# Kernel tuning notes

Hardware: AMD Instinct MI355X
Metric: run time of the kernel (lower is better)

## Reference

```python
import jax, jax.numpy as jnp
import numpy as np

H, D_MODEL, DK, DV = 16, 1024, 64, 64
B, S = 4, 2048
LN_EPS = 1e-6
NEG = -1e9


def setup_inputs() -> dict:
    key = jax.random.key(0)
    ks = jax.random.split(key, 8)
    query = jax.random.normal(ks[0], (B, S, D_MODEL), dtype=jnp.float32)
    k_in = jax.random.normal(ks[1], (B, S, D_MODEL), dtype=jnp.float32)
    v_in = jax.random.normal(ks[2], (B, S, D_MODEL), dtype=jnp.float32)
    mask = jax.random.randint(ks[3], (B, S, S), 0, 2, dtype=jnp.int32)
    sc = 1.0 / np.sqrt(D_MODEL)
    w_qs = jax.random.normal(ks[4], (D_MODEL, H * DK), dtype=jnp.float32) * sc
    w_ks = jax.random.normal(ks[5], (D_MODEL, H * DK), dtype=jnp.float32) * sc
    w_vs = jax.random.normal(ks[6], (D_MODEL, H * DV), dtype=jnp.float32) * sc
    w_out = jax.random.normal(ks[7], (H * DV, D_MODEL), dtype=jnp.float32) * (1.0 / np.sqrt(H * DV))
    ln_g = jnp.ones((D_MODEL,), dtype=jnp.float32)
    ln_b = jnp.zeros((D_MODEL,), dtype=jnp.float32)
    return {"query": query, "key": k_in, "value": v_in, "mask": mask,
            "w_qs": w_qs, "w_ks": w_ks, "w_vs": w_vs, "w_out": w_out,
            "ln_g": ln_g, "ln_b": ln_b}


def reference(query, key, value, mask, w_qs, w_ks, w_vs, w_out, ln_g, ln_b):
    # projections -> [B, H, S, dk/dv]
    q = (query @ w_qs).reshape(B, S, H, DK).transpose(0, 2, 1, 3)
    k = (key @ w_ks).reshape(B, S, H, DK).transpose(0, 2, 1, 3)
    v = (value @ w_vs).reshape(B, S, H, DV).transpose(0, 2, 1, 3)
    scores = jnp.einsum('bhqd,bhkd->bhqk', q, k) / np.sqrt(DK)
    scores = jnp.where(mask[:, None, :, :] == 0, NEG, scores)
    p = jax.nn.softmax(scores, axis=-1)  # dropout = identity in eval
    x = jnp.einsum('bhqk,bhkd->bhqd', p, v)  # [B,H,S,DV]
    x = x.transpose(0, 2, 1, 3).reshape(B, S, H * DV)
    out = x @ w_out + query  # dropout identity, residual
    mu = out.mean(-1, keepdims=True)
    var = out.var(-1, keepdims=True)
    return (out - mu) / jnp.sqrt(var + LN_EPS) * ln_g + ln_b
```

## Files before the change

### kernel.cpp

```cpp
#include <hip/hip_runtime.h>

#define BB   4
#define SS   2048
#define HH   16
#define DM   1024
#define DKV  64
#define LNEPS 1e-6f

#define MD_BF16 0
#define MD_F32  1
#define MD_F16  2

typedef __attribute__((ext_vector_type(8))) short bf16x8;
typedef __attribute__((ext_vector_type(4))) float f32x4;
#define MFMA16(a,b,c) __builtin_amdgcn_mfma_f32_16x16x32_bf16(a,b,c,0,0,0)

__device__ __forceinline__ float2 unpack2(unsigned int u) {
    union { unsigned int i; float f; } a, b;
    a.i = u << 16;
    b.i = u & 0xffff0000u;
    return make_float2(a.f, b.f);
}
__device__ __forceinline__ unsigned short f2bf(float f) {
    union { float f; unsigned int i; } c; c.f = f;
    unsigned int u = c.i;
    unsigned int r = u + 0x7fffu + ((u >> 16) & 1u);
    return (unsigned short)(r >> 16);
}
__device__ __forceinline__ unsigned short f2bf_t(float f) {
    union { float f; unsigned int i; } c; c.f = f;
    return (unsigned short)(c.i >> 16);
}
__device__ __forceinline__ float h2f(unsigned int bits16) {
    unsigned short s = (unsigned short)bits16;
    _Float16 x;
    __builtin_memcpy(&x, &s, 2);
    return (float)x;
}
__device__ __forceinline__ void load8m(const void* p, int mode, size_t e0, float* o) {
    if (mode == MD_F32) {
        const float* f = (const float*)p + e0;
        float4 a = *(const float4*)f;
        float4 b = *(const float4*)(f + 4);
        o[0] = a.x; o[1] = a.y; o[2] = a.z; o[3] = a.w;
        o[4] = b.x; o[5] = b.y; o[6] = b.z; o[7] = b.w;
    } else {
        uint4 u = *(const uint4*)((const ushort*)p + e0);
        unsigned v[4] = {u.x, u.y, u.z, u.w};
        if (mode == MD_BF16) {
#pragma unroll
            for (int j = 0; j < 4; ++j) { float2 t = unpack2(v[j]); o[2*j] = t.x; o[2*j+1] = t.y; }
        } else {
#pragma unroll
            for (int j = 0; j < 4; ++j) { o[2*j] = h2f(v[j] & 0xFFFFu); o[2*j+1] = h2f(v[j] >> 16); }
        }
    }
}
__device__ __forceinline__ void load4m(const void* p, int mode, size_t e0, float* o) {
    if (mode == MD_F32) {
        float4 v = *(const float4*)((const float*)p + e0);
        o[0] = v.x; o[1] = v.y; o[2] = v.z; o[3] = v.w;
    } else {
        uint2 u = *(const uint2*)((const ushort*)p + e0);
        if (mode == MD_BF16) {
            float2 a = unpack2(u.x), b = unpack2(u.y);
            o[0] = a.x; o[1] = a.y; o[2] = b.x; o[3] = b.y;
        } else {
            o[0] = h2f(u.x & 0xFFFFu); o[1] = h2f(u.x >> 16);
            o[2] = h2f(u.y & 0xFFFFu); o[3] = h2f(u.y >> 16);
        }
    }
}
__device__ __forceinline__ float loadS(const void* p, int mode, size_t i) {
    if (mode == MD_F32) return ((const float*)p)[i];
    unsigned short u = ((const ushort*)p)[i];
    if (mode == MD_BF16) { union { unsigned i; float f; } c; c.i = (unsigned)u << 16; return c.f; }
    return h2f(u);
}

struct SniffArgs { const void* p[10]; int nhalf[10]; };

__global__ void sniff_all(SniffArgs a, int* __restrict__ modes) {
    __shared__ int cE, cO;
    const int slots[9] = {0, 1, 2, 4, 5, 6, 7, 8, 9};
    const int slot = slots[blockIdx.x];
    const ushort* p = (const ushort*)a.p[slot];
    const int nhalf = a.nhalf[slot];
    if (threadIdx.x == 0) { cE = 0; cO = 0; }
    __syncthreads();
    int e = 0, o = 0;
    for (int i = threadIdx.x; i < nhalf; i += 256) {
        unsigned ex = (p[i] >> 7) & 0xFFu;
        int hit = (ex < 100u || ex == 0xFFu) ? 1 : 0;
        if (i & 1) o += hit; else e += hit;
    }
    atomicAdd(&cE, e);
    atomicAdd(&cO, o);
    __syncthreads();
    if (threadIdx.x == 0) {
        int total = cE + cO;
        modes[slot] = (total < 48) ? MD_BF16 : ((cO * 4 < cE) ? MD_F32 : MD_F16);
    }
}

__global__ __launch_bounds__(256) void mpack(
    const int* __restrict__ mask, unsigned int* __restrict__ pm)
{
    const int w = blockIdx.x * 256 + threadIdx.x;
    const int* p = mask + (size_t)w * 32;
    unsigned int bits = 0u;
#pragma unroll
    for (int j = 0; j < 8; ++j) {
        int4 v = *(const int4*)(p + j * 4);
        bits |= (v.x ? 1u : 0u) << (4 * j);
        bits |= (v.y ? 1u : 0u) << (4 * j + 1);
        bits |= (v.z ? 1u : 0u) << (4 * j + 2);
        bits |= (v.w ? 1u : 0u) << (4 * j + 3);
    }
    pm[w] = bits;
}

__global__ __launch_bounds__(256) void wtrans(
    const void* __restrict__ W, ushort* __restrict__ Wt,
    const int* __restrict__ modes, int wslot)
{
    __shared__ ushort T[64][68];
    const int tid = threadIdx.x;
    const int m = modes[wslot];
    const int k0 = blockIdx.y * 64, n0 = blockIdx.x * 64;

    const int r = tid >> 2, c = (tid & 3) * 16;
    float t[4];
#pragma unroll
    for (int j = 0; j < 4; ++j) {
        load4m(W, m, (size_t)(k0 + r) * DM + n0 + c + 4 * j, t);
#pragma unroll
        for (int i = 0; i < 4; ++i) T[r][c + 4 * j + i] = f2bf(t[i]);
    }
    __syncthreads();

    const int rn = tid >> 2, ck = (tid & 3) * 16;
    union { ushort u[8]; uint4 v; } p0, p1;
#pragma unroll
    for (int j = 0; j < 8; ++j) { p0.u[j] = T[ck + j][rn]; p1.u[j] = T[ck + 8 + j][rn]; }
    ushort* op = &Wt[(size_t)(n0 + rn) * DM + k0 + ck];
    *(uint4*)op = p0.v;
    *(uint4*)(op + 8) = p1.v;
}

__global__ __launch_bounds__(256) void proj_mfma(
    const void* __restrict__ Araw, const ushort* __restrict__ Wt,
    ushort* __restrict__ Out, const int* __restrict__ modes,
    int aslot, int vmode, float scale)
{
    __shared__ __align__(16) ushort As[128][40];
    __shared__ __align__(16) ushort Bs[128][40];

    const int tid = threadIdx.x;
    const int lane = tid & 63, wv = tid >> 6;
    const int quad = lane >> 4, L = lane & 15;
    const int m0 = blockIdx.y * 128, n0 = blockIdx.x * 128;
    const int wm = (wv >> 1) * 64, wn = (wv & 1) * 64;
    const int ma = modes[aslot];

    f32x4 acc[4][4];
#pragma unroll
    for (int i = 0; i < 4; ++i)
#pragma unroll
        for (int j = 0; j < 4; ++j) { acc[i][j][0] = 0.f; acc[i][j][1] = 0.f; acc[i][j][2] = 0.f; acc[i][j][3] = 0.f; }

    const int arow = tid >> 1, aseg = tid & 1;

    for (int kt = 0; kt < 32; ++kt) {
        const int k0 = kt * 32;
        {
            float t0[8], t1[8];
            load8m(Araw, ma, (size_t)(m0 + arow) * DM + k0 + aseg * 16, t0);
            load8m(Araw, ma, (size_t)(m0 + arow) * DM + k0 + aseg * 16 + 8, t1);
            union { ushort u[8]; uint4 v; } p0, p1;
#pragma unroll
            for (int j = 0; j < 8; ++j) { p0.u[j] = f2bf(t0[j]); p1.u[j] = f2bf(t1[j]); }
            *(uint4*)&As[arow][aseg * 16]     = p0.v;
            *(uint4*)&As[arow][aseg * 16 + 8] = p1.v;

            const ushort* wp = &Wt[(size_t)(n0 + arow) * DM + k0 + aseg * 16];
            *(uint4*)&Bs[arow][aseg * 16]     = *(const uint4*)wp;
            *(uint4*)&Bs[arow][aseg * 16 + 8] = *(const uint4*)(wp + 8);
        }
        __syncthreads();

        bf16x8 af[4], bfr[4];
#pragma unroll
        for (int tm = 0; tm < 4; ++tm) af[tm] = *(const bf16x8*)&As[wm + tm * 16 + L][quad * 8];
#pragma unroll
        for (int tn = 0; tn < 4; ++tn) bfr[tn] = *(const bf16x8*)&Bs[wn + tn * 16 + L][quad * 8];
#pragma unroll
        for (int tm = 0; tm < 4; ++tm)
#pragma unroll
            for (int tn = 0; tn < 4; ++tn)
                acc[tm][tn] = MFMA16(af[tm], bfr[tn], acc[tm][tn]);
        __syncthreads();
    }

#pragma unroll
    for (int tm = 0; tm < 4; ++tm)
#pragma unroll
        for (int tn = 0; tn < 4; ++tn)
#pragma unroll
            for (int r = 0; r < 4; ++r) {
                const int mm = m0 + wm + tm * 16 + quad * 4 + r;
                const int n = n0 + wn + tn * 16 + L;
                const int b = mm >> 11, s = mm & 2047;
                const int h = n >> 6, d = n & 63;
                const size_t o = vmode
                    ? ((size_t)(b * HH + h) * DKV + d) * SS + s
                    : ((size_t)(b * HH + h) * SS + s) * DKV + d;
                Out[o] = f2bf(acc[tm][tn][r] * scale);
            }
}

__global__ __launch_bounds__(256) void attn_mfma(
    const ushort* __restrict__ Q, const ushort* __restrict__ K,
    const ushort* __restrict__ Vt, const unsigned int* __restrict__ pm,
    ushort* __restrict__ Xo)
{
    __shared__ __align__(16) ushort Ks[64][72];
    __shared__ __align__(16) ushort Vs[64][72];
    __shared__ __align__(16) ushort Ps[64][72];

    const int tid = threadIdx.x;
    const int lane = tid & 63, wv = tid >> 6;
    const int quad = lane >> 4, L = lane & 15;
    const int bh = blockIdx.y, b = bh >> 4, h = bh & 15;
    const int q0 = blockIdx.x * 64;

    const ushort* qp = &Q[((size_t)bh * SS + q0 + wv * 16 + L) * DKV + quad * 8];
    const bf16x8 aq0 = *(const bf16x8*)qp;
    const bf16x8 aq1 = *(const bf16x8*)(qp + 32);

    f32x4 O[4];
    float lacc[4];
#pragma unroll
    for (int t = 0; t < 4; ++t) { O[t][0] = 0.f; O[t][1] = 0.f; O[t][2] = 0.f; O[t][3] = 0.f; }
#pragma unroll
    for (int r = 0; r < 4; ++r) lacc[r] = 0.f;

    const int sr = tid >> 2, sg = tid & 3;
    const ushort* kbase = &K[((size_t)bh * SS + sr) * DKV + sg * 16];
    const ushort* vbase = &Vt[((size_t)bh * DKV + sr) * SS + sg * 16];
    const unsigned int* pmr[4];
#pragma unroll
    for (int r = 0; r < 4; ++r)
        pmr[r] = pm + ((size_t)b * SS + q0 + wv * 16 + quad * 4 + r) * 64;

    for (int kt = 0; kt < 32; ++kt) {
        __syncthreads();
        *(uint4*)&Ks[sr][sg * 16]     = *(const uint4*)kbase;
        *(uint4*)&Ks[sr][sg * 16 + 8] = *(const uint4*)(kbase + 8);
        *(uint4*)&Vs[sr][sg * 16]     = *(const uint4*)vbase;
        *(uint4*)&Vs[sr][sg * 16 + 8] = *(const uint4*)(vbase + 8);
        kbase += 64 * DKV;
        vbase += 64;

        uint2 mw[4];
#pragma unroll
        for (int r = 0; r < 4; ++r) mw[r] = *(const uint2*)(pmr[r] + 2 * kt);

        __syncthreads();

        f32x4 sc[4];
#pragma unroll
        for (int t = 0; t < 4; ++t) {
            bf16x8 b0 = *(const bf16x8*)&Ks[t * 16 + L][quad * 8];
            bf16x8 b1 = *(const bf16x8*)&Ks[t * 16 + L][32 + quad * 8];
            f32x4 c; c[0] = 0.f; c[1] = 0.f; c[2] = 0.f; c[3] = 0.f;
            c = MFMA16(aq0, b0, c);
            c = MFMA16(aq1, b1, c);
            sc[t] = c;
        }

#pragma unroll
        for (int r = 0; r < 4; ++r) {
            const unsigned mx = mw[r].x, my = mw[r].y;
#pragma unroll
            for (int t = 0; t < 4; ++t) {
                const float s = fminf(sc[t][r], 30.f);
                const float e = __expf(s);
                const unsigned wsel = (t & 2) ? my : mx;
                const float p = ((wsel >> ((t & 1) * 16 + L)) & 1u) ? e : 0.f;
                lacc[r] += p;
                Ps[wv * 16 + quad * 4 + r][t * 16 + L] = f2bf_t(p);
            }
        }

        bf16x8 ap0 = *(const bf16x8*)&Ps[wv * 16 + L][quad * 8];
        bf16x8 ap1 = *(const bf16x8*)&Ps[wv * 16 + L][32 + quad * 8];
#pragma unroll
        for (int t = 0; t < 4; ++t) {
            bf16x8 v0 = *(const bf16x8*)&Vs[t * 16 + L][quad * 8];
            bf16x8 v1 = *(const bf16x8*)&Vs[t * 16 + L][32 + quad * 8];
            O[t] = MFMA16(ap0, v0, O[t]);
            O[t] = MFMA16(ap1, v1, O[t]);
        }
    }

    float inv[4];
#pragma unroll
    for (int r = 0; r < 4; ++r) {
        float l = lacc[r];
#pragma unroll
        for (int off = 1; off < 16; off <<= 1) l += __shfl_xor(l, off, 64);
        inv[r] = 1.f / l;
    }
#pragma unroll
    for (int t = 0; t < 4; ++t)
#pragma unroll
        for (int r = 0; r < 4; ++r) {
            const int qg = q0 + wv * 16 + quad * 4 + r;
            Xo[((size_t)b * SS + qg) * DM + h * DKV + t * 16 + L] = f2bf(O[t][r] * inv[r]);
        }
}

__global__ __launch_bounds__(256) void oproj_mfma(
    const ushort* __restrict__ Xin, const ushort* __restrict__ Wt,
    const void* __restrict__ Qres, float* __restrict__ Out,
    const int* __restrict__ modes)
{
    __shared__ __align__(16) ushort As[128][40];
    __shared__ __align__(16) ushort Bs[128][40];

    const int tid = threadIdx.x;
    const int lane = tid & 63, wv = tid >> 6;
    const int quad = lane >> 4, L = lane & 15;
    const int m0 = blockIdx.y * 128, n0 = blockIdx.x * 128;
    const int wm = (wv >> 1) * 64, wn = (wv & 1) * 64;
    const int mq = modes[0];

    f32x4 acc[4][4];
#pragma unroll
    for (int i = 0; i < 4; ++i)
#pragma unroll
        for (int j = 0; j < 4; ++j) { acc[i][j][0] = 0.f; acc[i][j][1] = 0.f; acc[i][j][2] = 0.f; acc[i][j][3] = 0.f; }

    const int arow = tid >> 1, aseg = tid & 1;

    for (int kt = 0; kt < 32; ++kt) {
        const int k0 = kt * 32;
        {
            const ushort* xp = &Xin[(size_t)(m0 + arow) * DM + k0 + aseg * 16];
            *(uint4*)&As[arow][aseg * 16]     = *(const uint4*)xp;
            *(uint4*)&As[arow][aseg * 16 + 8] = *(const uint4*)(xp + 8);
            const ushort* wp = &Wt[(size_t)(n0 + arow) * DM + k0 + aseg * 16];
            *(uint4*)&Bs[arow][aseg * 16]     = *(const uint4*)wp;
            *(uint4*)&Bs[arow][aseg * 16 + 8] = *(const uint4*)(wp + 8);
        }
        __syncthreads();

        bf16x8 af[4], bfr[4];
#pragma unroll
        for (int tm = 0; tm < 4; ++tm) af[tm] = *(const bf16x8*)&As[wm + tm * 16 + L][quad * 8];
#pragma unroll
        for (int tn = 0; tn < 4; ++tn) bfr[tn] = *(const bf16x8*)&Bs[wn + tn * 16 + L][quad * 8];
#pragma unroll
        for (int tm = 0; tm < 4; ++tm)
#pragma unroll
            for (int tn = 0; tn < 4; ++tn)
                acc[tm][tn] = MFMA16(af[tm], bfr[tn], acc[tm][tn]);
        __syncthreads();
    }

#pragma unroll
    for (int tm = 0; tm < 4; ++tm)
#pragma unroll
        for (int tn = 0; tn < 4; ++tn)
#pragma unroll
            for (int r = 0; r < 4; ++r) {
                const int mm = m0 + wm + tm * 16 + quad * 4 + r;
                const int n = n0 + wn + tn * 16 + L;
                const size_t idx = (size_t)mm * DM + n;
                Out[idx] = acc[tm][tn][r] + loadS(Qres, mq, idx);
            }
}

__global__ __launch_bounds__(256) void ln_k(
    float* __restrict__ Out, const void* __restrict__ G,
    const void* __restrict__ Bt, const int* __restrict__ modes)
{
    const int tid = threadIdx.x, wv = tid >> 6, lane = tid & 63;
    const int row = blockIdx.x * 4 + wv;
    const int mg = modes[8], mb = modes[9];
    const size_t base = (size_t)row * DM + lane * 16;

    float v[16];
    float s = 0.f, q = 0.f;
#pragma unroll
    for (int j = 0; j < 16; j += 4) {
        float4 t = *(const float4*)&Out[base + j];
        v[j] = t.x; v[j+1] = t.y; v[j+2] = t.z; v[j+3] = t.w;
        s += t.x + t.y + t.z + t.w;
        q += t.x*t.x + t.y*t.y + t.z*t.z + t.w*t.w;
    }
#pragma unroll
    for (int off = 1; off < 64; off <<= 1) {
        s += __shfl_xor(s, off, 64);
        q += __shfl_xor(q, off, 64);
    }
    const float mu = s * (1.f / 1024.f);
    const float var = q * (1.f / 1024.f) - mu * mu;
    const float inv = rsqrtf(var + LNEPS);

    float gj[16], bj[16];
#pragma unroll
    for (int j = 0; j < 16; j += 4) {
        load4m(G,  mg, (size_t)lane * 16 + j, gj + j);
        load4m(Bt, mb, (size_t)lane * 16 + j, bj + j);
    }
#pragma unroll
    for (int j = 0; j < 16; j += 4) {
        float4 o;
        o.x = (v[j]   - mu) * inv * gj[j]   + bj[j];
        o.y = (v[j+1] - mu) * inv * gj[j+1] + bj[j+1];
        o.z = (v[j+2] - mu) * inv * gj[j+2] + bj[j+2];
        o.w = (v[j+3] - mu) * inv * gj[j+3] + bj[j+3];
        *(float4*)&Out[base + j] = o;
    }
}

extern "C" void kernel_launch(void* const* d_in, const int* in_sizes, int n_in,
                              void* d_out, int out_size, void* d_ws, size_t ws_size,
                              hipStream_t stream)
{
    const void* query = d_in[0];
    const void* key_i = d_in[1];
    const void* value = d_in[2];
    const int*  mask  = (const int*)d_in[3];
    const void* w_qs  = d_in[4];
    const void* w_ks  = d_in[5];
    const void* w_vs  = d_in[6];
    const void* w_out = d_in[7];
    const void* ln_g  = d_in[8];
    const void* ln_b  = d_in[9];
    float* out = (float*)d_out;

    int* modes = (int*)d_ws;
    const size_t PE = (size_t)BB * HH * SS * DKV;
    ushort* Qw = (ushort*)((char*)d_ws + 256);
    ushort* Kw = Qw + PE;
    ushort* Vw = Kw + PE;
    ushort* Xw = Vw + PE;
    ushort* Wt  = Xw;
    ushort* Wt2 = Qw;
    unsigned int* pmask = (unsigned int*)d_out;

    SniffArgs sa;
    for (int i = 0; i < 10; ++i) {
        sa.p[i] = d_in[i];
        sa.nhalf[i] = in_sizes[i] < 4096 ? in_sizes[i] : 4096;
    }
    sniff_all<<<9, 256, 0, stream>>>(sa, modes);
    mpack<<<2048, 256, 0, stream>>>(mask, pmask);

    dim3 gproj(8, 64), gtr(16, 16);

    wtrans<<<gtr, 256, 0, stream>>>(w_qs, Wt, modes, 4);
    proj_mfma<<<gproj, 256, 0, stream>>>(query, Wt, Qw, modes, 0, 0, 0.125f);
    wtrans<<<gtr, 256, 0, stream>>>(w_ks, Wt, modes, 5);
    proj_mfma<<<gproj, 256, 0, stream>>>(key_i, Wt, Kw, modes, 1, 0, 1.0f);
    wtrans<<<gtr, 256, 0, stream>>>(w_vs, Wt, modes, 6);
    proj_mfma<<<gproj, 256, 0, stream>>>(value, Wt, Vw, modes, 2, 1, 1.0f);

    attn_mfma<<<dim3(32, 64), 256, 0, stream>>>(Qw, Kw, Vw, pmask, Xw);

    wtrans<<<gtr, 256, 0, stream>>>(w_out, Wt2, modes, 7);
    oproj_mfma<<<gproj, 256, 0, stream>>>(Xw, Wt2, query, out, modes);
    ln_k<<<2048, 256, 0, stream>>>(out, ln_g, ln_b, modes);
}
```

Before: 586.5 us.

## Pre-convert projection inputs to bf16 and load GEMM tiles via global_load_lds

Adds a standalone conversion kernel that casts each activation input to bf16 in a scratch buffer, so the projection GEMM reads bf16 instead of converting fp32 on the fly. Both projection and output GEMMs now fill shared memory with direct global-to-LDS 16-byte loads and an unpadded 32-wide tile layout. This removes register staging and conversion work from the GEMM inner loop. In exchange it adds an extra read/write pass per input, may introduce LDS bank conflicts now that padding is gone, and relocates the weight transpose buffer into the output region.

After: 536.4 us. 1.09x faster.

```diff
diff --git a/kernel.cpp b/kernel.cpp
--- a/kernel.cpp
+++ b/kernel.cpp
@@ -14,6 +14,12 @@
 typedef __attribute__((ext_vector_type(8))) short bf16x8;
 typedef __attribute__((ext_vector_type(4))) float f32x4;
 #define MFMA16(a,b,c) __builtin_amdgcn_mfma_f32_16x16x32_bf16(a,b,c,0,0,0)
+
+__device__ __forceinline__ void gl_lds16(const ushort* g, ushort* l) {
+    __builtin_amdgcn_global_load_lds(
+        (const __attribute__((address_space(1))) void*)g,
+        (__attribute__((address_space(3))) void*)l, 16, 0, 0);
+}
 
 __device__ __forceinline__ float2 unpack2(unsigned int u) {
     union { unsigned int i; float f; } a, b;
@@ -120,6 +126,22 @@
     pm[w] = bits;
 }
 
+__global__ __launch_bounds__(256) void aconv(
+    const void* __restrict__ A, ushort* __restrict__ Ab,
+    const int* __restrict__ modes, int slot)
+{
+    const int m = modes[slot];
+    const size_t e0 = ((size_t)blockIdx.x * 256 + threadIdx.x) * 16;
+    float t[16];
+    load8m(A, m, e0, t);
+    load8m(A, m, e0 + 8, t + 8);
+    union { ushort u[16]; uint4 v[2]; } p;
+#pragma unroll
+    for (int j = 0; j < 16; ++j) p.u[j] = f2bf(t[j]);
+    *(uint4*)&Ab[e0]     = p.v[0];
+    *(uint4*)&Ab[e0 + 8] = p.v[1];
+}
+
 __global__ __launch_bounds__(256) void wtrans(
     const void* __restrict__ W, ushort* __restrict__ Wt,
     const int* __restrict__ modes, int wslot)
@@ -149,51 +171,44 @@
 }
 
 __global__ __launch_bounds__(256) void proj_mfma(
-    const void* __restrict__ Araw, const ushort* __restrict__ Wt,
-    ushort* __restrict__ Out, const int* __restrict__ modes,
-    int aslot, int vmode, float scale)
-{
-    __shared__ __align__(16) ushort As[128][40];
-    __shared__ __align__(16) ushort Bs[128][40];
+    const ushort* __restrict__ A, const ushort* __restrict__ Wt,
+    ushort* __restrict__ Out, int vmode, float scale)
+{
+    __shared__ __align__(16) ushort Asf[128 * 32];
+    __shared__ __align__(16) ushort Bsf[128 * 32];
 
     const int tid = threadIdx.x;
     const int lane = tid & 63, wv = tid >> 6;
     const int quad = lane >> 4, L = lane & 15;
     const int m0 = blockIdx.y * 128, n0 = blockIdx.x * 128;
     const int wm = (wv >> 1) * 64, wn = (wv & 1) * 64;
-    const int ma = modes[aslot];
+
+    const int e0 = (wv * 2 + 0) * 512 + lane * 8;
+    const int e1 = (wv * 2 + 1) * 512 + lane * 8;
+    const ushort* gA0 = A  + (size_t)(m0 + (e0 >> 5)) * DM + (e0 & 31);
+    const ushort* gA1 = A  + (size_t)(m0 + (e1 >> 5)) * DM + (e1 & 31);
+    const ushort* gB0 = Wt + (size_t)(n0 + (e0 >> 5)) * DM + (e0 & 31);
+    const ushort* gB1 = Wt + (size_t)(n0 + (e1 >> 5)) * DM + (e1 & 31);
 
     f32x4 acc[4][4];
 #pragma unroll
     for (int i = 0; i < 4; ++i)
 #pragma unroll
         for (int j = 0; j < 4; ++j) { acc[i][j][0] = 0.f; acc[i][j][1] = 0.f; acc[i][j][2] = 0.f; acc[i][j][3] = 0.f; }
-
-    const int arow = tid >> 1, aseg = tid & 1;
 
     for (int kt = 0; kt < 32; ++kt) {
         const int k0 = kt * 32;
-        {
-            float t0[8], t1[8];
-            load8m(Araw, ma, (size_t)(m0 + arow) * DM + k0 + aseg * 16, t0);
-            load8m(Araw, ma, (size_t)(m0 + arow) * DM + k0 + aseg * 16 + 8, t1);
-            union { ushort u[8]; uint4 v; } p0, p1;
-#pragma unroll
-            for (int j = 0; j < 8; ++j) { p0.u[j] = f2bf(t0[j]); p1.u[j] = f2bf(t1[j]); }
-            *(uint4*)&As[arow][aseg * 16]     = p0.v;
-            *(uint4*)&As[arow][aseg * 16 + 8] = p1.v;
-
-            const ushort* wp = &Wt[(size_t)(n0 + arow) * DM + k0 + aseg * 16];
-            *(uint4*)&Bs[arow][aseg * 16]     = *(const uint4*)wp;
-            *(uint4*)&Bs[arow][aseg * 16 + 8] = *(const uint4*)(wp + 8);
-        }
+        gl_lds16(gA0 + k0, &Asf[e0]);
+        gl_lds16(gA1 + k0, &Asf[e1]);
+        gl_lds16(gB0 + k0, &Bsf[e0]);
+        gl_lds16(gB1 + k0, &Bsf[e1]);
         __syncthreads();
 
         bf16x8 af[4], bfr[4];
 #pragma unroll
-        for (int tm = 0; tm < 4; ++tm) af[tm] = *(const bf16x8*)&As[wm + tm * 16 + L][quad * 8];
-#pragma unroll
-        for (int tn = 0; tn < 4; ++tn) bfr[tn] = *(const bf16x8*)&Bs[wn + tn * 16 + L][quad * 8];
+        for (int tm = 0; tm < 4; ++tm) af[tm] = *(const bf16x8*)&Asf[(wm + tm * 16 + L) * 32 + quad * 8];
+#pragma unroll
+        for (int tn = 0; tn < 4; ++tn) bfr[tn] = *(const bf16x8*)&Bsf[(wn + tn * 16 + L) * 32 + quad * 8];
 #pragma unroll
         for (int tm = 0; tm < 4; ++tm)
 #pragma unroll
@@ -326,8 +341,8 @@
     const void* __restrict__ Qres, float* __restrict__ Out,
     const int* __restrict__ modes)
 {
-    __shared__ __align__(16) ushort As[128][40];
-    __shared__ __align__(16) ushort Bs[128][40];
+    __shared__ __align__(16) ushort Asf[128 * 32];
+    __shared__ __align__(16) ushort Bsf[128 * 32];
 
     const int tid = threadIdx.x;
     const int lane = tid & 63, wv = tid >> 6;
@@ -336,31 +351,32 @@
     const int wm = (wv >> 1) * 64, wn = (wv & 1) * 64;
     const int mq = modes[0];
 
+    const int e0 = (wv * 2 + 0) * 512 + lane * 8;
+    const int e1 = (wv * 2 + 1) * 512 + lane * 8;
+    const ushort* gA0 = Xin + (size_t)(m0 + (e0 >> 5)) * DM + (e0 & 31);
+    const ushort* gA1 = Xin + (size_t)(m0 + (e1 >> 5)) * DM + (e1 & 31);
+    const ushort* gB0 = Wt  + (size_t)(n0 + (e0 >> 5)) * DM + (e0 & 31);
+    const ushort* gB1 = Wt  + (size_t)(n0 + (e1 >> 5)) * DM + (e1 & 31);
+
     f32x4 acc[4][4];
 #pragma unroll
     for (int i = 0; i < 4; ++i)
 #pragma unroll
         for (int j = 0; j < 4; ++j) { acc[i][j][0] = 0.f; acc[i][j][1] = 0.f; acc[i][j][2] = 0.f; acc[i][j][3] = 0.f; }
-
-    const int arow = tid >> 1, aseg = tid & 1;
 
     for (int kt = 0; kt < 32; ++kt) {
         const int k0 = kt * 32;
-        {
-            const ushort* xp = &Xin[(size_t)(m0 + arow) * DM + k0 + aseg * 16];
-            *(uint4*)&As[arow][aseg * 16]     = *(const uint4*)xp;
-            *(uint4*)&As[arow][aseg * 16 + 8] = *(const uint4*)(xp + 8);
-            const ushort* wp = &Wt[(size_t)(n0 + arow) * DM + k0 + aseg * 16];
-            *(uint4*)&Bs[arow][aseg * 16]     = *(const uint4*)wp;
-            *(uint4*)&Bs[arow][aseg * 16 + 8] = *(const uint4*)(wp + 8);
-        }
+        gl_lds16(gA0 + k0, &Asf[e0]);
+        gl_lds16(gA1 + k0, &Asf[e1]);
+        gl_lds16(gB0 + k0, &Bsf[e0]);
+        gl_lds16(gB1 + k0, &Bsf[e1]);
         __syncthreads();
 
         bf16x8 af[4], bfr[4];
 #pragma unroll
-        for (int tm = 0; tm < 4; ++tm) af[tm] = *(const bf16x8*)&As[wm + tm * 16 + L][quad * 8];
-#pragma unroll
-        for (int tn = 0; tn < 4; ++tn) bfr[tn] = *(const bf16x8*)&Bs[wn + tn * 16 + L][quad * 8];
+        for (int tm = 0; tm < 4; ++tm) af[tm] = *(const bf16x8*)&Asf[(wm + tm * 16 + L) * 32 + quad * 8];
+#pragma unroll
+        for (int tn = 0; tn < 4; ++tn) bfr[tn] = *(const bf16x8*)&Bsf[(wn + tn * 16 + L) * 32 + quad * 8];
 #pragma unroll
         for (int tm = 0; tm < 4; ++tm)
 #pragma unroll
@@ -448,8 +464,9 @@
     ushort* Kw = Qw + PE;
     ushort* Vw = Kw + PE;
     ushort* Xw = Vw + PE;
-    ushort* Wt  = Xw;
-    ushort* Wt2 = Qw;
+    ushort* Abuf = Xw;
+    ushort* Wt   = (ushort*)((char*)d_out + (4 << 20));
+    ushort* Wt2  = Qw;
     unsigned int* pmask = (unsigned int*)d_out;
 
     SniffArgs sa;
@@ -463,11 +480,16 @@
     dim3 gproj(8, 64), gtr(16, 16);
 
     wtrans<<<gtr, 256, 0, stream>>>(w_qs, Wt, modes, 4);
-    proj_mfma<<<gproj, 256, 0, stream>>>(query, Wt, Qw, modes, 0, 0, 0.125f);
+    aconv<<<2048, 256, 0, stream>>>(query, Abuf, modes, 0);
+    proj_mfma<<<gproj, 256, 0, stream>>>(Abuf, Wt, Qw, 0, 0.125f);
+
     wtrans<<<gtr, 256, 0, stream>>>(w_ks, Wt, modes, 5);
-    proj_mfma<<<gproj, 256, 0, stream>>>(key_i, Wt, Kw, modes, 1, 0, 1.0f);
+    aconv<<<2048, 256, 0, stream>>>(key_i, Abuf, modes, 1);
+    proj_mfma<<<gproj, 256, 0, stream>>>(Abuf, Wt, Kw, 0, 1.0f);
+
     wtrans<<<gtr, 256, 0, stream>>>(w_vs, Wt, modes, 6);
-    proj_mfma<<<gproj, 256, 0, stream>>>(value, Wt, Vw, modes, 2, 1, 1.0f);
+    aconv<<<2048, 256, 0, stream>>>(value, Abuf, modes, 2);
+    proj_mfma<<<gproj, 256, 0, stream>>>(Abuf, Wt, Vw, 1, 1.0f);
 
     attn_mfma<<<dim3(32, 64), 256, 0, stream>>>(Qw, Kw, Vw, pmask, Xw);
 
```
